# Kernel optimization log

Measured on AMD Instinct MI355X. Metric: run time of the kernel, lower is better.

The kernel has to match this reference:

```python
import jax, jax.numpy as jnp
import numpy as np


def setup_inputs() -> dict:
    key = jax.random.key(0)
    k1, k2, k3, k4, k5 = jax.random.split(key, 5)
    B, IN_N, POSE = 32, 8192, 64
    M = 8                     # matrix_pose_dim = sqrt(64)
    NH, S2, HID = 32, 256, 256  # in_n/(img^2), img^2, hidden_dim
    OUT_N = 64
    return {
        "current_pose": jax.random.normal(k1, (B, IN_N, POSE), jnp.float32),
        "w_current": 0.02 * jax.random.normal(k2, (1, 1, IN_N, M, M), jnp.float32),
        "w_next": 0.02 * jax.random.normal(k3, (OUT_N, M, M), jnp.float32),
        "E_proj": 0.02 * jax.random.normal(k4, (NH, S2, HID), jnp.float32),
        "rel_embedd": jax.random.normal(k5, (1, 1, POSE), jnp.float32),
    }


def reference(current_pose, w_current, w_next, E_proj, rel_embedd):
    B, IN_N, POSE = current_pose.shape
    M = w_current.shape[-1]           # matrix_pose_dim
    NH, S2, HID = E_proj.shape        # heads, img*img, hidden_dim
    OUT_N = w_next.shape[0]

    # w_current: (1,1,IN_N,M,M) -> (1,IN_N,M,M); per-capsule pose-matrix multiply
    wc = w_current.reshape(IN_N, M, M)[None]
    cp = current_pose.reshape(B, IN_N, M, M)
    cp = jnp.matmul(cp, wc)                      # (B, IN_N, M, M)

    # raw reshape (row-major, matches torch .reshape) then Linformer projection
    cp = cp.reshape(B, POSE, NH, 1, S2)
    cp = jnp.matmul(cp, E_proj)                  # (B, POSE, NH, 1, HID)
    cp = cp[:, :, :, 0, :]                       # squeeze(3) -> (B, POSE, NH, HID)
    cp = cp.reshape(B, NH * HID, POSE)           # raw reshape as in torch

    # dots = softmax over out_n axis of a constant tensor == uniform 1/OUT_N.
    # einsum('bij,bje->bie') with uniform dots == mean over j, broadcast over i.
    pooled = jnp.sum(cp, axis=1, keepdims=True) / OUT_N   # (B, 1, POSE)
    npc = jnp.broadcast_to(pooled, (B, OUT_N, POSE))

    # add relative embedding (h_out = w_out = output_img_size = 1)
    npc = npc.reshape(B, OUT_N, 1, 1, POSE) + rel_embedd  # (B,OUT_N,1,1,POSE)
    npc = jnp.transpose(npc, (0, 2, 3, 1, 4)).reshape(B, OUT_N, POSE)

    # next-layer pose-matrix multiply
    npc = npc.reshape(B, OUT_N, M, M)
    npc = jnp.matmul(npc, w_next[None])           # (B, OUT_N, M, M)
    npc = npc.reshape(B, 1, 1, OUT_N, POSE)
    return npc[:, 0]                              # squeeze(1) -> (B,1,OUT_N,POSE)
```

## Files before the change

kernel.cpp:

```cpp
#include <hip/hip_runtime.h>
#include <hip/hip_bf16.h>


typedef short short8_t __attribute__((ext_vector_type(8)));
typedef float f32x4_t __attribute__((ext_vector_type(4)));
typedef int   int4_t  __attribute__((ext_vector_type(4)));

__device__ __forceinline__ short f2bf(float f) {
    union { float f; unsigned u; } v; v.f = f;
    unsigned r = v.u + 0x7FFFu + ((v.u >> 16) & 1u);
    return (short)(r >> 16);
}

__device__ __forceinline__ int cvt_pk(float x, float y) {
    int r;
    asm("v_cvt_pk_bf16_f32 %0, %1, %2" : "=v"(r) : "v"(x), "v"(y));
    return r;
}

__global__ void k_prep(const float* __restrict__ WC, short* __restrict__ WCf,
                       const float* __restrict__ E, float* __restrict__ F) {
    if (blockIdx.x < 256) {
        int t   = blockIdx.x * 256 + threadIdx.x;
        int l   = t & 63;
        int pc  = (t >> 6) & 15;
        int rp  = t >> 10;
        int lhi = l >> 4;
        int j   = l & 15;
        int row = (pc * 4 + lhi) * 128 + rp * 2 + (j >> 3);
        const float* src = WC + ((size_t)row << 6) + (j & 7);
        short8_t o;
        #pragma unroll
        for (int k = 0; k < 8; ++k) o[k] = f2bf(src[k * 8]);
        ((short8_t*)WCf)[t] = o;
    } else {
        int idx = ((blockIdx.x - 256) * 256 + threadIdx.x) * 4;
        int q   = idx & 63;
        int row = idx >> 6;
        int r   = row >> 6;
        int e   = row & 63;
        int nh  = r >> 2;
        int s2  = ((r & 3) << 6) + e;
        const float* base = E + (((size_t)nh * 256 + s2) << 8) + q;
        float4 s0 = *(const float4*)(base);
        float4 s1 = *(const float4*)(base + 64);
        float4 s2v = *(const float4*)(base + 128);
        float4 s3 = *(const float4*)(base + 192);
        float4 o;
        o.x = s0.x + s1.x + s2v.x + s3.x;
        o.y = s0.y + s1.y + s2v.y + s3.y;
        o.z = s0.z + s1.z + s2v.z + s3.z;
        o.w = s0.w + s1.w + s2v.w + s3.w;
        *(float4*)(F + idx) = o;
    }
}

__global__ void __launch_bounds__(512, 4)
k_bc(const float* __restrict__ CP, const short* __restrict__ WCf,
     const float* __restrict__ F, float* __restrict__ P) {
    int gx   = blockIdx.x;
    int half = gx & 1;
    int rpg  = gx >> 1;
    int b0   = blockIdx.y * 2;
    int w = threadIdx.x >> 6;
    int l = threadIdx.x & 63;
    int b_loc  = w & 1;
    int rp_loc = w >> 1;
    int rp = rpg * 4 + rp_loc;
    int r0 = rp * 2;
    int b  = b0 + b_loc;

    int i16   = l & 15;
    int r_sel = i16 >> 3;
    int m1    = i16 & 7;
    int lhi   = l >> 4;

    __shared__ float gbuf[8][2048];
    __shared__ float Stile[2][512];
    __shared__ float redp[8][2][64];

    const float* cp_base = CP + ((size_t)b << 19) + ((size_t)(r0 + r_sel) << 6) + m1 * 8;
    const short8_t* wf   = (const short8_t*)WCf + (size_t)rp * 1024 + (half * 8) * 64 + l;

    short8_t wr0 = wf[0 * 64], wr1 = wf[1 * 64], wr2 = wf[2 * 64], wr3 = wf[3 * 64];
    short8_t wr4 = wf[4 * 64], wr5 = wf[5 * 64], wr6 = wf[6 * 64], wr7 = wf[7 * 64];
    asm volatile("" :: "v"(wr0), "v"(wr1), "v"(wr2), "v"(wr3),
                       "v"(wr4), "v"(wr5), "v"(wr6), "v"(wr7));
    asm volatile("s_waitcnt vmcnt(0)" ::: "memory");
    __builtin_amdgcn_sched_barrier(0);

    int wu = __builtin_amdgcn_readfirstlane(w);
    float* gb = &gbuf[wu][0];

    const float* pbase = cp_base + (((size_t)(half * 8) * 4 + lhi) << 13);
    #define CPA(c) (pbase + ((size_t)((c) * 4) << 13))

    #define ISSUE(c, off) do {                                                        \
        __builtin_amdgcn_global_load_lds((const void*)(CPA(c)),                       \
                                         (void*)(gb + (off)), 16, 0, 0);              \
        __builtin_amdgcn_global_load_lds((const void*)(CPA(c) + 4),                   \
                                         (void*)(gb + (off) + 256), 16, 0, 0);        \
    } while (0)

    #define WAITVM(N) do {                                                            \
        asm volatile("s_waitcnt vmcnt(" #N ")" ::: "memory");                         \
        __builtin_amdgcn_sched_barrier(0);                                            \
    } while (0)

    f32x4_t acc0 = {0.f, 0.f, 0.f, 0.f};
    f32x4_t acc1 = {0.f, 0.f, 0.f, 0.f};

    #define COMPUTE(off, wfr, accX) do {                                              \
        float4 x0 = *(const float4*)(gb + (off) + (size_t)l * 4);                     \
        float4 x1 = *(const float4*)(gb + (off) + 256 + (size_t)l * 4);               \
        int4_t ai;                                                                    \
        ai[0] = cvt_pk(x0.x, x0.y); ai[1] = cvt_pk(x0.z, x0.w);                       \
        ai[2] = cvt_pk(x1.x, x1.y); ai[3] = cvt_pk(x1.z, x1.w);                       \
        accX = __builtin_amdgcn_mfma_f32_16x16x32_bf16(                               \
            __builtin_bit_cast(short8_t, ai), wfr, accX, 0, 0, 0);                    \
    } while (0)

    ISSUE(0, 0);    ISSUE(1, 512);
    ISSUE(2, 1024); ISSUE(3, 1536);
    WAITVM(4);
    COMPUTE(0, wr0, acc0); COMPUTE(512, wr1, acc1);
    __builtin_amdgcn_sched_barrier(0);
    ISSUE(4, 0);    ISSUE(5, 512);
    WAITVM(4);
    COMPUTE(1024, wr2, acc0); COMPUTE(1536, wr3, acc1);
    __builtin_amdgcn_sched_barrier(0);
    ISSUE(6, 1024); ISSUE(7, 1536);
    WAITVM(4);
    COMPUTE(0, wr4, acc0); COMPUTE(512, wr5, acc1);
    WAITVM(0);
    COMPUTE(1024, wr6, acc0); COMPUTE(1536, wr7, acc1);

    #undef COMPUTE
    #undef WAITVM
    #undef ISSUE
    #undef CPA

    f32x4_t acc;
    #pragma unroll
    for (int v = 0; v < 4; ++v) acc[v] = acc0[v] + acc1[v];

    int col = i16;
    #pragma unroll
    for (int v = 0; v < 4; ++v) {
        int row = lhi * 4 + v;
        if (row < 8 && col < 8)
            Stile[b_loc][rp_loc * 128 + row * 8 + col] = acc[v];
        else if (row >= 8 && col >= 8)
            Stile[b_loc][rp_loc * 128 + 64 + (row - 8) * 8 + (col - 8)] = acc[v];
    }
    __syncthreads();

    int g  = l >> 4;
    int ql = l & 15;
    const float* Fb = F + (((size_t)(rpg * 512 + w * 64 + g)) << 6) + ql * 4;
    f32x4_t p0 = {0.f, 0.f, 0.f, 0.f};
    f32x4_t p1 = {0.f, 0.f, 0.f, 0.f};
    #pragma unroll 4
    for (int s = 0; s < 16; ++s) {
        int jl = w * 64 + s * 4 + g;
        float4 fv = *(const float4*)(Fb + ((size_t)(s * 4) << 6));
        float s0 = Stile[0][jl];
        float s1 = Stile[1][jl];
        p0[0] += s0 * fv.x; p0[1] += s0 * fv.y; p0[2] += s0 * fv.z; p0[3] += s0 * fv.w;
        p1[0] += s1 * fv.x; p1[1] += s1 * fv.y; p1[2] += s1 * fv.z; p1[3] += s1 * fv.w;
    }
    #pragma unroll
    for (int c = 0; c < 4; ++c) {
        p0[c] += __shfl_xor(p0[c], 16, 64);
        p0[c] += __shfl_xor(p0[c], 32, 64);
        p1[c] += __shfl_xor(p1[c], 16, 64);
        p1[c] += __shfl_xor(p1[c], 32, 64);
    }
    if (l < 16) {
        *(f32x4_t*)(&redp[w][0][ql * 4]) = p0;
        *(f32x4_t*)(&redp[w][1][ql * 4]) = p1;
    }
    __syncthreads();

    if (threadIdx.x < 128) {
        int bb = threadIdx.x >> 6;
        int q  = threadIdx.x & 63;
        float s = 0.f;
        #pragma unroll
        for (int ww = 0; ww < 8; ++ww) s += redp[ww][bb][q];
        P[((size_t)((b0 + bb) * 32 + gx) << 6) + q] = s;
    }
}

__global__ void k_final(const float* __restrict__ P, const float* __restrict__ rel,
                        const float* __restrict__ WN, float* __restrict__ out) {
    int b  = blockIdx.x;
    int oc = blockIdx.y;
    int t  = threadIdx.x;
    int q    = t & 63;
    int sgrp = t >> 6;
    const float* Pb = P + ((size_t)(b * 32) << 6);
    float s = 0.f;
    #pragma unroll
    for (int c = sgrp * 8; c < sgrp * 8 + 8; ++c)
        s += Pb[((size_t)c << 6) + q];
    __shared__ float red[4][64];
    red[sgrp][q] = s;
    __syncthreads();
    __shared__ float pool_s[64];
    if (t < 64) {
        pool_s[t] = (red[0][t] + red[1][t] + red[2][t] + red[3][t]) * (1.0f / 64.0f)
                    + rel[t];
    }
    __syncthreads();
    #pragma unroll
    for (int idx = t; idx < 1024; idx += 256) {
        int o = oc * 16 + (idx >> 6);
        int e = idx & 63;
        int m1 = e >> 3, m2 = e & 7;
        float a = 0.f;
        #pragma unroll
        for (int k = 0; k < 8; ++k)
            a += pool_s[m1 * 8 + k] * WN[o * 64 + k * 8 + m2];
        out[((size_t)b << 12) + o * 64 + e] = a;
    }
}

extern "C" void kernel_launch(void* const* d_in, const int* in_sizes, int n_in,
                              void* d_out, int out_size, void* d_ws, size_t ws_size,
                              hipStream_t stream) {
    const float* current_pose = (const float*)d_in[0];
    const float* w_current    = (const float*)d_in[1];
    const float* w_next       = (const float*)d_in[2];
    const float* E_proj       = (const float*)d_in[3];
    const float* rel_embedd   = (const float*)d_in[4];
    float* out = (float*)d_out;

    char* ws = (char*)d_ws;
    float* F   = (float*)(ws);
    short* WCf = (short*)(ws + (2u << 20));
    float* P   = (float*)(ws + (3u << 20));

    k_prep<<<dim3(768), dim3(256), 0, stream>>>(w_current, WCf, E_proj, F);
    k_bc<<<dim3(32, 16), dim3(512), 0, stream>>>(current_pose, WCf, F, P);
    k_final<<<dim3(32, 4), dim3(256), 0, stream>>>(P, rel_embedd, w_next, out);
}
```

Baseline: 27.31 us.

## Share cooperative coalesced LDS staging of input tiles across waves with block barriers

Replaces per-wave private LDS buffers filled with scattered 16-byte gathers by a block-shared double buffer. All eight waves cooperatively load contiguous 1KB row segments, and each wave then reads its operand slice from the shared tile. The goal is better global-load coalescing and a smaller LDS footprint, which could raise occupancy. In exchange it adds block-wide s_barrier synchronisation between the load and compute stages, and padding is used to limit LDS bank conflicts.

```diff
diff --git a/kernel.cpp b/kernel.cpp
--- a/kernel.cpp
+++ b/kernel.cpp
@@ -67,7 +67,6 @@
     int b_loc  = w & 1;
     int rp_loc = w >> 1;
     int rp = rpg * 4 + rp_loc;
-    int r0 = rp * 2;
     int b  = b0 + b_loc;
 
     int i16   = l & 15;
@@ -75,12 +74,11 @@
     int m1    = i16 & 7;
     int lhi   = l >> 4;
 
-    __shared__ float gbuf[8][2048];
+    __shared__ float Abuf[2][16][528];
     __shared__ float Stile[2][512];
     __shared__ float redp[8][2][64];
 
-    const float* cp_base = CP + ((size_t)b << 19) + ((size_t)(r0 + r_sel) << 6) + m1 * 8;
-    const short8_t* wf   = (const short8_t*)WCf + (size_t)rp * 1024 + (half * 8) * 64 + l;
+    const short8_t* wf = (const short8_t*)WCf + (size_t)rp * 1024 + (half * 8) * 64 + l;
 
     short8_t wr0 = wf[0 * 64], wr1 = wf[1 * 64], wr2 = wf[2 * 64], wr3 = wf[3 * 64];
     short8_t wr4 = wf[4 * 64], wr5 = wf[5 * 64], wr6 = wf[6 * 64], wr7 = wf[7 * 64];
@@ -89,17 +87,17 @@
     asm volatile("s_waitcnt vmcnt(0)" ::: "memory");
     __builtin_amdgcn_sched_barrier(0);
 
-    int wu = __builtin_amdgcn_readfirstlane(w);
-    float* gb = &gbuf[wu][0];
-
-    const float* pbase = cp_base + (((size_t)(half * 8) * 4 + lhi) << 13);
-    #define CPA(c) (pbase + ((size_t)((c) * 4) << 13))
-
-    #define ISSUE(c, off) do {                                                        \
-        __builtin_amdgcn_global_load_lds((const void*)(CPA(c)),                       \
-                                         (void*)(gb + (off)), 16, 0, 0);              \
-        __builtin_amdgcn_global_load_lds((const void*)(CPA(c) + 4),                   \
-                                         (void*)(gb + (off) + 256), 16, 0, 0);        \
+    #define ISSUE4(ks, X) do {                                                        \
+        _Pragma("unroll")                                                             \
+        for (int k = 0; k < 4; ++k) {                                                 \
+            int g  = w * 4 + k;                                                       \
+            int bg = g >> 4, pi = (g >> 1) & 7, hg = g & 1;                           \
+            const float* s_ = CP + ((size_t)(b0 + bg) << 19)                          \
+                + ((size_t)((half * 32 + (ks) * 8 + pi) * 128 + rpg * 8) << 6)        \
+                + hg * 256 + l * 4;                                                   \
+            __builtin_amdgcn_global_load_lds((const void*)s_,                         \
+                (void*)(&Abuf[X][bg * 8 + pi][hg * 256]), 16, 0, 0);                  \
+        }                                                                             \
     } while (0)
 
     #define WAITVM(N) do {                                                            \
@@ -107,38 +105,52 @@
         __builtin_amdgcn_sched_barrier(0);                                            \
     } while (0)
 
+    #define RBAR() do {                                                               \
+        asm volatile("s_barrier" ::: "memory");                                       \
+        __builtin_amdgcn_sched_barrier(0);                                            \
+    } while (0)
+
     f32x4_t acc0 = {0.f, 0.f, 0.f, 0.f};
     f32x4_t acc1 = {0.f, 0.f, 0.f, 0.f};
 
-    #define COMPUTE(off, wfr, accX) do {                                              \
-        float4 x0 = *(const float4*)(gb + (off) + (size_t)l * 4);                     \
-        float4 x1 = *(const float4*)(gb + (off) + 256 + (size_t)l * 4);               \
-        int4_t ai;                                                                    \
+    #define COMPUTE2(ks, X, wlo, whi) do {                                            \
+        const float* a0p = &Abuf[X][b_loc * 8 + 0 * 4 + lhi]                          \
+                                  [(rp_loc * 2 + r_sel) * 64 + m1 * 8];               \
+        const float* a1p = &Abuf[X][b_loc * 8 + 1 * 4 + lhi]                          \
+                                  [(rp_loc * 2 + r_sel) * 64 + m1 * 8];               \
+        float4 x0 = *(const float4*)(a0p);                                            \
+        float4 x1 = *(const float4*)(a0p + 4);                                        \
+        float4 y0 = *(const float4*)(a1p);                                            \
+        float4 y1 = *(const float4*)(a1p + 4);                                        \
+        int4_t ai, bi;                                                                \
         ai[0] = cvt_pk(x0.x, x0.y); ai[1] = cvt_pk(x0.z, x0.w);                       \
         ai[2] = cvt_pk(x1.x, x1.y); ai[3] = cvt_pk(x1.z, x1.w);                       \
-        accX = __builtin_amdgcn_mfma_f32_16x16x32_bf16(                               \
-            __builtin_bit_cast(short8_t, ai), wfr, accX, 0, 0, 0);                    \
-    } while (0)
-
-    ISSUE(0, 0);    ISSUE(1, 512);
-    ISSUE(2, 1024); ISSUE(3, 1536);
-    WAITVM(4);
-    COMPUTE(0, wr0, acc0); COMPUTE(512, wr1, acc1);
-    __builtin_amdgcn_sched_barrier(0);
-    ISSUE(4, 0);    ISSUE(5, 512);
-    WAITVM(4);
-    COMPUTE(1024, wr2, acc0); COMPUTE(1536, wr3, acc1);
-    __builtin_amdgcn_sched_barrier(0);
-    ISSUE(6, 1024); ISSUE(7, 1536);
-    WAITVM(4);
-    COMPUTE(0, wr4, acc0); COMPUTE(512, wr5, acc1);
-    WAITVM(0);
-    COMPUTE(1024, wr6, acc0); COMPUTE(1536, wr7, acc1);
-
-    #undef COMPUTE
+        bi[0] = cvt_pk(y0.x, y0.y); bi[1] = cvt_pk(y0.z, y0.w);                       \
+        bi[2] = cvt_pk(y1.x, y1.y); bi[3] = cvt_pk(y1.z, y1.w);                       \
+        acc0 = __builtin_amdgcn_mfma_f32_16x16x32_bf16(                               \
+            __builtin_bit_cast(short8_t, ai), wlo, acc0, 0, 0, 0);                    \
+        acc1 = __builtin_amdgcn_mfma_f32_16x16x32_bf16(                               \
+            __builtin_bit_cast(short8_t, bi), whi, acc1, 0, 0, 0);                    \
+    } while (0)
+
+    ISSUE4(0, 0); ISSUE4(1, 1);
+    WAITVM(4); RBAR();
+    COMPUTE2(0, 0, wr0, wr1);
+    RBAR();
+    ISSUE4(2, 0);
+    WAITVM(4); RBAR();
+    COMPUTE2(1, 1, wr2, wr3);
+    RBAR();
+    ISSUE4(3, 1);
+    WAITVM(4); RBAR();
+    COMPUTE2(2, 0, wr4, wr5);
+    WAITVM(0); RBAR();
+    COMPUTE2(3, 1, wr6, wr7);
+
+    #undef COMPUTE2
+    #undef RBAR
     #undef WAITVM
-    #undef ISSUE
-    #undef CPA
+    #undef ISSUE4
 
     f32x4_t acc;
     #pragma unroll
```

New measurement: 29.12 us. 1.07x slower.
